# Performance work log

Measured on AMD Instinct MI355X. Metric: run time of the kernel, lower is better.

Reference implementation:

```python
import jax, jax.numpy as jnp
import numpy as np

MANIFOLD_K = 1.0   # Lorentz curvature manifold.k
POWER_K = 2        # power_k
EPS_PHI = 1e-6
EPS_FP = 1e-8

N, IN_C, OUT_C, H = 32768, 128, 128, 8


def setup_inputs() -> dict:
    key = jax.random.key(0)
    ks = jax.random.split(key, 11)
    s = 1.0 / np.sqrt(IN_C)  # nn.Linear default init scale
    u = lambda k, shape: jax.random.uniform(k, shape, jnp.float32, -s, s)
    return {
        "query_input": jax.random.normal(ks[0], (N, IN_C), jnp.float32),
        "source_input": jax.random.normal(ks[1], (N, IN_C), jnp.float32),
        "Wq_w": u(ks[2], (H, OUT_C, IN_C)),
        "Wq_b": u(ks[3], (H, OUT_C)),
        "Wk_w": u(ks[4], (H, OUT_C, IN_C)),
        "Wk_b": u(ks[5], (H, OUT_C)),
        "Wv_w": u(ks[6], (H, OUT_C, IN_C)),
        "Wv_b": u(ks[7], (H, OUT_C)),
        "v_map_w": u(ks[8], (OUT_C, OUT_C)),  # v_map_mlp acts on v (out_channels feats)
        "v_map_b": u(ks[9], (OUT_C,)),
        "norm_scale": jnp.ones((), jnp.float32),
    }


def _fp(x, p):
    # norm(x) / (norm(x**p) + eps) * x**p, norms over last dim
    norm_x = jnp.linalg.norm(x, axis=-1, keepdims=True)
    xp = x ** p
    norm_xp = jnp.linalg.norm(xp, axis=-1, keepdims=True)
    return norm_x / (norm_xp + EPS_FP) * xp


def reference(query_input, source_input, Wq_w, Wq_b, Wk_w, Wk_b, Wv_w, Wv_b,
              v_map_w, v_map_b, norm_scale):
    # Per-head HypLinear space part; the concatenated time coordinate is
    # immediately stripped by hyp_*[..., 1:] in linear_focus_attention,
    # so only the linear (space) output participates in the math.
    qs = jnp.einsum('ni,hoi->nho', query_input, Wq_w) + Wq_b   # [N,H,D]
    ks_ = jnp.einsum('ni,hoi->nho', source_input, Wk_w) + Wk_b  # [N,H,D]
    v = jnp.einsum('ni,hoi->nho', source_input, Wv_w) + Wv_b    # [N,H,D]

    denom_scale = jnp.abs(norm_scale) + EPS_PHI
    phi_qs = _fp((jax.nn.relu(qs) + EPS_PHI) / denom_scale, POWER_K)
    phi_ks = _fp((jax.nn.relu(ks_) + EPS_PHI) / denom_scale, POWER_K)

    k_transpose_v = jnp.einsum('nhm,nhd->hmd', phi_ks, v)        # [H,D,D]
    numerator = jnp.einsum('nhm,hmd->nhd', phi_qs, k_transpose_v)
    denominator = jnp.einsum('nhd,hd->nh', phi_qs, phi_ks.sum(axis=0))[..., None]
    attn_output = numerator / (denominator + EPS_PHI)            # [N,H,D]

    vss = jnp.einsum('nhd,od->nho', v, v_map_w) + v_map_b        # v_map_mlp(v)
    attn_output = attn_output + vss

    out = attn_output.mean(axis=1)                               # heads mean [N,D]
    out_time = jnp.sqrt(jnp.sum(out ** 2, axis=-1, keepdims=True) + MANIFOLD_K)
    return jnp.concatenate([out_time, out], axis=-1)             # [N,D+1]
```

## Files before the change

### kernel.cpp

```cpp
#include <hip/hip_runtime.h>

#define NTOK   32768
#define CDIM   128
#define NH     8
#define QT     32

typedef __bf16 bf16;
typedef __bf16 bf16x4v __attribute__((ext_vector_type(4)));
typedef __bf16 bf16x8v __attribute__((ext_vector_type(8)));
typedef float  f32x4   __attribute__((ext_vector_type(4)));

__device__ __forceinline__ f32x4 mfma16(bf16x8v a, bf16x8v b, f32x4 c) {
  return __builtin_amdgcn_mfma_f32_16x16x32_bf16(a, b, c, 0, 0, 0);
}

__device__ __forceinline__ float xred16(float v) {
  v += __shfl_xor(v, 1);
  v += __shfl_xor(v, 2);
  v += __shfl_xor(v, 4);
  v += __shfl_xor(v, 8);
  return v;
}

template<int CTRL>
__device__ __forceinline__ float dpp_add(float x) {
  int y = __builtin_amdgcn_mov_dpp(__float_as_int(x), CTRL, 0xf, 0xf, true);
  return x + __int_as_float(y);
}
__device__ __forceinline__ float xred16d(float v) {
  v = dpp_add<0xB1>(v);
  v = dpp_add<0x4E>(v);
  v = dpp_add<0x141>(v);
  v = dpp_add<0x140>(v);
  return v;
}

__device__ __forceinline__ int sidx(int row, int col) {
  return row * 128 + (col ^ ((row & 7) << 3));
}

__device__ __forceinline__ int tidx(int h, int tile, int kk, int lane) {
  return (((h * 8 + tile) * 4 + kk) * 64 + lane) * 8;
}

__global__ void __launch_bounds__(256) k_prepA(
    const float* __restrict__ src,
    const float* __restrict__ Wq, const float* __restrict__ Wk,
    const float* __restrict__ Wv, const float* __restrict__ Wv_b,
    bf16* __restrict__ srcT,
    bf16* __restrict__ wqT, bf16* __restrict__ wkT, bf16* __restrict__ wvT,
    float* __restrict__ Wvs, float* __restrict__ Wvbs)
{
  const int bid = blockIdx.x;
  const int tid = threadIdx.x;
  if (bid < 2048) {
    const int rb = bid;
    const int row = tid >> 4, col0 = (tid & 15) * 8;
    const float* p = src + (rb * 16 + row) * CDIM + col0;
    f32x4 v0 = *(const f32x4*)p;
    f32x4 v1 = *(const f32x4*)(p + 4);
    bf16x8v o;
    o[0] = (bf16)v0[0]; o[1] = (bf16)v0[1]; o[2] = (bf16)v0[2]; o[3] = (bf16)v0[3];
    o[4] = (bf16)v1[0]; o[5] = (bf16)v1[1]; o[6] = (bf16)v1[2]; o[7] = (bf16)v1[3];
    const int kk = col0 >> 5, lg = (col0 >> 3) & 3;
    const int lane = row + 16 * lg;
    *(bf16x8v*)(srcT + ((rb * 4 + kk) * 64 + lane) * 8) = o;
  } else {
    const int b = bid - 2048;
    const int h = b >> 6;
    const int o = (b & 63) * 2 + (tid >> 7);
    const int i = tid & 127;
    const int s = (h * CDIM + o) * CDIM + i;
    const int ot = o >> 4, l15 = o & 15;
    const int kk = i >> 5, lg = (i >> 3) & 3, j = i & 7;
    const int dst = tidx(h, ot, kk, l15 + 16 * lg) + j;
    wqT[dst] = (bf16)Wq[s];
    wkT[dst] = (bf16)Wk[s];
    wvT[dst] = (bf16)Wv[s];
    if (h == 0) {
      float sm = 0.f;
#pragma unroll
      for (int hh = 0; hh < NH; ++hh) sm += Wv[(hh * CDIM + o) * CDIM + i];
      Wvs[o * CDIM + i] = sm;
      if (o == 0) {
        float sb = 0.f;
#pragma unroll
        for (int hh = 0; hh < NH; ++hh) sb += Wv_b[hh * CDIM + i];
        Wvbs[i] = sb;
      }
    }
  }
}

__global__ void __launch_bounds__(256, 2) k_ktv(
    const bf16* __restrict__ srcT,
    const bf16* __restrict__ wkT, const bf16* __restrict__ wvT,
    const float* __restrict__ Wk_b, const float* __restrict__ Wv_b,
    bf16* __restrict__ ktv_part, float* __restrict__ ksum_part,
    int nsub, int cpx )
{
  const int x = blockIdx.x & 7;
  const int g = blockIdx.x >> 3;
  const int c = x * cpx + (g >> 3);
  const int h = g & 7;

  const int tid = threadIdx.x;
  const int w = tid >> 6, l = tid & 63;
  const int l15 = l & 15, lg = l >> 4;
  const int os = w * 32, owt = os >> 4;

  __shared__ bf16 s_phiT[128][68];
  __shared__ bf16 s_vT[128][68];
  __shared__ float s_red2[8][64];
  __shared__ float s_scale[64];

  const f32x4 z4 = {0.f, 0.f, 0.f, 0.f};

  bf16x8v bWk[2][4], bWv[2][4];
  float bK[2], bV[2];
#pragma unroll
  for (int ot = 0; ot < 2; ++ot) {
#pragma unroll
    for (int kk = 0; kk < 4; ++kk) {
      bWk[ot][kk] = *(const bf16x8v*)(wkT + tidx(h, owt + ot, kk, l));
      bWv[ot][kk] = *(const bf16x8v*)(wvT + tidx(h, owt + ot, kk, l));
    }
    bK[ot] = Wk_b[h * CDIM + os + ot * 16 + l15];
    bV[ot] = Wv_b[h * CDIM + os + ot * 16 + l15];
  }

  const int wd = (w >> 1) * 64, wm = (w & 1) * 64;
  f32x4 acc[4][4];
#pragma unroll
  for (int dt = 0; dt < 4; ++dt)
#pragma unroll
    for (int mt = 0; mt < 4; ++mt) acc[dt][mt] = z4;
  float ksacc[2] = {0.f, 0.f};

#pragma unroll 1
  for (int s = 0; s < nsub; ++s) {
    const int rbase = (c * nsub + s) * 4;
    f32x4 accK[4][2], accV[4][2];
#pragma unroll
    for (int nt = 0; nt < 4; ++nt)
#pragma unroll
      for (int ot = 0; ot < 2; ++ot) { accK[nt][ot] = z4; accV[nt][ot] = z4; }
#pragma unroll
    for (int kk = 0; kk < 4; ++kk) {
      bf16x8v a[4];
#pragma unroll
      for (int nt = 0; nt < 4; ++nt)
        a[nt] = *(const bf16x8v*)(srcT + (((rbase + nt) * 4 + kk) * 64 + l) * 8);
#pragma unroll
      for (int nt = 0; nt < 4; ++nt)
#pragma unroll
        for (int ot = 0; ot < 2; ++ot) {
          accK[nt][ot] = mfma16(a[nt], bWk[ot][kk], accK[nt][ot]);
          accV[nt][ot] = mfma16(a[nt], bWv[ot][kk], accV[nt][ot]);
        }
    }
    bf16x4v vq[4][2];
#pragma unroll
    for (int nt = 0; nt < 4; ++nt)
#pragma unroll
      for (int ot = 0; ot < 2; ++ot)
#pragma unroll
        for (int r = 0; r < 4; ++r)
          vq[nt][ot][r] = (bf16)(accV[nt][ot][r] + bV[ot]);
#pragma unroll
    for (int nt = 0; nt < 4; ++nt)
#pragma unroll
      for (int r = 0; r < 4; ++r) {
        float a2 = 0.f, a4 = 0.f;
#pragma unroll
        for (int ot = 0; ot < 2; ++ot) {
          float xv = fmaxf(accK[nt][ot][r] + bK[ot], 0.f) + 1e-6f;
          float x2 = xv * xv;
          accK[nt][ot][r] = x2;
          a2 += x2;
          a4 += x2 * x2;
        }
        a2 = xred16d(a2);
        a4 = xred16d(a4);
        if (l15 == 0) {
          s_red2[w * 2 + 0][nt * 16 + lg * 4 + r] = a2;
          s_red2[w * 2 + 1][nt * 16 + lg * 4 + r] = a4;
        }
      }
    __syncthreads();
    {
      float S2 = s_red2[0][l] + s_red2[2][l] + s_red2[4][l] + s_red2[6][l];
      float S4 = s_red2[1][l] + s_red2[3][l] + s_red2[5][l] + s_red2[7][l];
      s_scale[l] = sqrtf(S2) / (sqrtf(S4) + 1e-8f);
    }
#pragma unroll
    for (int nt = 0; nt < 4; ++nt) {
      f32x4 sc = *(const f32x4*)&s_scale[nt * 16 + lg * 4];
#pragma unroll
      for (int ot = 0; ot < 2; ++ot) {
        bf16x4v ph;
#pragma unroll
        for (int r = 0; r < 4; ++r) {
          float p = accK[nt][ot][r] * sc[r];
          ksacc[ot] += p;
          ph[r] = (bf16)p;
        }
        const int colb = os + ot * 16 + l15;
        *(bf16x4v*)&s_phiT[colb][nt * 16 + lg * 4] = ph;
        *(bf16x4v*)&s_vT[colb][nt * 16 + lg * 4] = vq[nt][ot];
      }
    }
    __syncthreads();
#pragma unroll
    for (int kkn = 0; kkn < 2; ++kkn) {
      bf16x8v aV[4], bP[4];
#pragma unroll
      for (int dt = 0; dt < 4; ++dt)
        aV[dt] = *(const bf16x8v*)&s_vT[wd + dt * 16 + l15][kkn * 32 + lg * 8];
#pragma unroll
      for (int mt = 0; mt < 4; ++mt)
        bP[mt] = *(const bf16x8v*)&s_phiT[wm + mt * 16 + l15][kkn * 32 + lg * 8];
#pragma unroll
      for (int dt = 0; dt < 4; ++dt)
#pragma unroll
        for (int mt = 0; mt < 4; ++mt)
          acc[dt][mt] = mfma16(aV[dt], bP[mt], acc[dt][mt]);
    }
  }

#pragma unroll
  for (int ot = 0; ot < 2; ++ot) {
    ksacc[ot] += __shfl_xor(ksacc[ot], 16);
    ksacc[ot] += __shfl_xor(ksacc[ot], 32);
  }
  if (l < 16) {
#pragma unroll
    for (int ot = 0; ot < 2; ++ot)
      ksum_part[(c * NH + h) * CDIM + os + ot * 16 + l] = ksacc[ot];
  }
  bf16* kp = ktv_part + ((c * NH + h) * 4 + w) * 4096;
#pragma unroll
  for (int dt = 0; dt < 4; ++dt)
#pragma unroll
    for (int mt = 0; mt < 4; ++mt) {
      bf16x4v q;
#pragma unroll
      for (int r = 0; r < 4; ++r) q[r] = (bf16)acc[dt][mt][r];
      *(bf16x4v*)(kp + ((dt * 4 + mt) * 64 + l) * 4) = q;
    }
}

__global__ void __launch_bounds__(256) k_finishB(
    const bf16* __restrict__ ktv_part, const float* __restrict__ ksum_part,
    const float* __restrict__ vmw, const float* __restrict__ vmb,
    const float* __restrict__ Wvs, const float* __restrict__ Wvbs,
    bf16* __restrict__ ktvT, bf16* __restrict__ ksb,
    bf16* __restrict__ w2sT, float* __restrict__ b2s, int nchunk)
{
  const int b = blockIdx.x;
  if (b < 512) {
    const int t = b * 256 + threadIdx.x;
    const int h = t >> 14;
    const int rem = t & 16383;
    const int d = rem >> 7, m = rem & 127;
    const int wq = ((d >> 6) << 1) | (m >> 6);
    const int dd = d & 63, mm = m & 63;
    const int dt = dd >> 4, r = dd & 3, lgp = (dd >> 2) & 3;
    const int mt = mm >> 4, l15p = mm & 15;
    const int lane = lgp * 16 + l15p;
    const int off = (h * 4 + wq) * 4096 + ((dt * 4 + mt) * 64 + lane) * 4 + r;
    float a = 0.f;
    for (int c = 0; c < nchunk; ++c)
      a += (float)ktv_part[c * (NH * 4 * 4096) + off];
    const int dtile = d >> 4, dl15 = d & 15;
    const int kk = m >> 5, mlg = (m >> 3) & 3, j = m & 7;
    ktvT[tidx(h, dtile, kk, dl15 + 16 * mlg) + j] = (bf16)a;
  } else if (b < 576) {
    const int t = (b - 512) * 256 + threadIdx.x;
    const int h = t >> 11;
    const int rem = t & 2047;
    const int kk = rem >> 9, lane = (rem >> 3) & 63, j = rem & 7;
    const int l15 = lane & 15, lg = lane >> 4;
    float a = 0.f;
    if (l15 == 0) {
      const int m = 32 * kk + 8 * lg + j;
      for (int c = 0; c < nchunk; ++c) a += ksum_part[(c * NH + h) * CDIM + m];
    }
    ksb[t] = (bf16)a;
  } else {
    const int sub = threadIdx.x >> 7, i = threadIdx.x & 127;
    const int o = (b - 576) * 2 + sub;
    __shared__ float s_vm[2][128];
    __shared__ float s_rd[2][128];
    s_vm[sub][i] = vmw[o * CDIM + i];
    __syncthreads();
    float acc = 0.f;
    for (int d = 0; d < CDIM; ++d) acc = fmaf(s_vm[sub][d], Wvs[d * CDIM + i], acc);
    const int ot = o >> 4, l15 = o & 15;
    const int kk = i >> 5, lg = (i >> 3) & 3, j = i & 7;
    w2sT[tidx(0, ot, kk, l15 + 16 * lg) + j] = (bf16)acc;
    s_rd[sub][i] = s_vm[sub][i] * Wvbs[i];
    __syncthreads();
    for (int st = 64; st > 0; st >>= 1) {
      if (i < st) s_rd[sub][i] += s_rd[sub][i + st];
      __syncthreads();
    }
    if (i == 0) b2s[o] = s_rd[sub][0] + 8.f * vmb[o];
  }
}

__global__ void __launch_bounds__(256, 2) k_out(
    const float* __restrict__ query, const bf16* __restrict__ srcT,
    const bf16* __restrict__ wqT, const float* __restrict__ Wq_b,
    const bf16* __restrict__ ktvT, const bf16* __restrict__ ksb,
    const bf16* __restrict__ w2sT, const float* __restrict__ b2s,
    float* __restrict__ out)
{
  const int nb = blockIdx.x * QT;
  const int tid = threadIdx.x;
  const int w = tid >> 6, l = tid & 63;
  const int l15 = l & 15, lg = l >> 4;
  const int os = w * 32, owt = os >> 4;

  __shared__ bf16 s_q[QT * 128];
  __shared__ bf16 s_phi[2][QT * 128];
  __shared__ float s_time[4][QT] __attribute__((aligned(16)));

  const f32x4 z4 = {0.f, 0.f, 0.f, 0.f};

#pragma unroll
  for (int j = 0; j < 4; ++j) {
    const int flat = tid + j * 256;
    const int n = flat >> 5, c4 = (flat & 31) * 4;
    f32x4 vq = *(const f32x4*)(query + (nb + n) * CDIM + c4);
    bf16x4v bq;
    bq[0] = (bf16)vq[0]; bq[1] = (bf16)vq[1]; bq[2] = (bf16)vq[2]; bq[3] = (bf16)vq[3];
    *(bf16x4v*)&s_q[sidx(n, c4)] = bq;
  }

  f32x4 accO[2][2];
#pragma unroll
  for (int nt = 0; nt < 2; ++nt)
#pragma unroll
    for (int ot = 0; ot < 2; ++ot) accO[nt][ot] = z4;

  __syncthreads();

  bf16x8v aq[2][4];
#pragma unroll
  for (int nt = 0; nt < 2; ++nt)
#pragma unroll
    for (int kk = 0; kk < 4; ++kk)
      aq[nt][kk] = *(const bf16x8v*)&s_q[sidx(nt * 16 + l15, kk * 32 + lg * 8)];

  for (int h = 0; h < NH; ++h) {
    bf16x8v wf[2][4], kf[2][4], kt[4];
#pragma unroll
    for (int ot = 0; ot < 2; ++ot)
#pragma unroll
      for (int kk = 0; kk < 4; ++kk) {
        wf[ot][kk] = *(const bf16x8v*)(wqT + tidx(h, owt + ot, kk, l));
        kf[ot][kk] = *(const bf16x8v*)(ktvT + tidx(h, owt + ot, kk, l));
      }
#pragma unroll
    for (int kk = 0; kk < 4; ++kk)
      kt[kk] = *(const bf16x8v*)(ksb + ((h * 4 + kk) * 64 + l) * 8);
    float bQ[2];
#pragma unroll
    for (int ot = 0; ot < 2; ++ot) bQ[ot] = Wq_b[h * CDIM + os + ot * 16 + l15];

    f32x4 accQ[2][2];
#pragma unroll
    for (int nt = 0; nt < 2; ++nt)
#pragma unroll
      for (int ot = 0; ot < 2; ++ot) accQ[nt][ot] = z4;
#pragma unroll
    for (int kk = 0; kk < 4; ++kk)
#pragma unroll
      for (int ot = 0; ot < 2; ++ot)
#pragma unroll
        for (int nt = 0; nt < 2; ++nt)
          accQ[nt][ot] = mfma16(aq[nt][kk], wf[ot][kk], accQ[nt][ot]);

    bf16* ph = s_phi[h & 1];
#pragma unroll
    for (int nt = 0; nt < 2; ++nt)
#pragma unroll
      for (int ot = 0; ot < 2; ++ot)
#pragma unroll
        for (int r = 0; r < 4; ++r) {
          float x = fmaxf(accQ[nt][ot][r] + bQ[ot], 0.f) + 1e-6f;
          ph[sidx(nt * 16 + lg * 4 + r, os + ot * 16 + l15)] = (bf16)(x * x);
        }
    __syncthreads();

    bf16x8v ap[2][4];
#pragma unroll
    for (int nt = 0; nt < 2; ++nt)
#pragma unroll
      for (int kk = 0; kk < 4; ++kk)
        ap[nt][kk] = *(const bf16x8v*)&ph[sidx(nt * 16 + l15, kk * 32 + lg * 8)];

    f32x4 accN[2][2], accT[2];
#pragma unroll
    for (int nt = 0; nt < 2; ++nt) {
      accT[nt] = z4;
#pragma unroll
      for (int dt = 0; dt < 2; ++dt) accN[nt][dt] = z4;
    }
#pragma unroll
    for (int kk = 0; kk < 4; ++kk) {
#pragma unroll
      for (int dt = 0; dt < 2; ++dt)
#pragma unroll
        for (int nt = 0; nt < 2; ++nt)
          accN[nt][dt] = mfma16(ap[nt][kk], kf[dt][kk], accN[nt][dt]);
#pragma unroll
      for (int nt = 0; nt < 2; ++nt)
        accT[nt] = mfma16(ap[nt][kk], kt[kk], accT[nt]);
    }
#pragma unroll
    for (int nt = 0; nt < 2; ++nt)
#pragma unroll
      for (int r = 0; r < 4; ++r) {
        float tr = __shfl(accT[nt][r], l & 48);
        float m = 1.0f / tr;
#pragma unroll
        for (int dt = 0; dt < 2; ++dt)
          accO[nt][dt][r] = fmaf(accN[nt][dt][r], m, accO[nt][dt][r]);
      }
  }

  const int rb0 = blockIdx.x * 2;
#pragma unroll
  for (int kk = 0; kk < 4; ++kk) {
    bf16x8v a[2];
#pragma unroll
    for (int nt = 0; nt < 2; ++nt)
      a[nt] = *(const bf16x8v*)(srcT + (((rb0 + nt) * 4 + kk) * 64 + l) * 8);
#pragma unroll
    for (int ot = 0; ot < 2; ++ot) {
      bf16x8v bw = *(const bf16x8v*)(w2sT + tidx(0, owt + ot, kk, l));
#pragma unroll
      for (int nt = 0; nt < 2; ++nt)
        accO[nt][ot] = mfma16(a[nt], bw, accO[nt][ot]);
    }
  }
  float bb[2];
#pragma unroll
  for (int ot = 0; ot < 2; ++ot) bb[ot] = b2s[os + ot * 16 + l15];

  float ps[2][4];
#pragma unroll
  for (int nt = 0; nt < 2; ++nt)
#pragma unroll
    for (int r = 0; r < 4; ++r) ps[nt][r] = 0.f;
#pragma unroll
  for (int nt = 0; nt < 2; ++nt)
#pragma unroll
    for (int ot = 0; ot < 2; ++ot)
#pragma unroll
      for (int r = 0; r < 4; ++r) {
        float v = (accO[nt][ot][r] + bb[ot]) * 0.125f;
        accO[nt][ot][r] = v;
        ps[nt][r] += v * v;
      }
#pragma unroll
  for (int nt = 0; nt < 2; ++nt)
#pragma unroll
    for (int r = 0; r < 4; ++r) {
      float t = xred16d(ps[nt][r]);
      if (l15 == 0) s_time[w][nt * 16 + lg * 4 + r] = t;
    }
#pragma unroll
  for (int nt = 0; nt < 2; ++nt)
#pragma unroll
    for (int ot = 0; ot < 2; ++ot)
#pragma unroll
      for (int r = 0; r < 4; ++r)
        out[(nb + nt * 16 + lg * 4 + r) * 129 + 1 + os + ot * 16 + l15] = accO[nt][ot][r];
  __syncthreads();
  if (tid < QT) {
    float S = 1.0f + s_time[0][tid] + s_time[1][tid] + s_time[2][tid] + s_time[3][tid];
    out[(nb + tid) * 129] = sqrtf(S);
  }
}

extern "C" void kernel_launch(void* const* d_in, const int* in_sizes, int n_in,
                              void* d_out, int out_size, void* d_ws, size_t ws_size,
                              hipStream_t stream) {
  const float* query  = (const float*)d_in[0];
  const float* source = (const float*)d_in[1];
  const float* Wq_w   = (const float*)d_in[2];
  const float* Wq_b   = (const float*)d_in[3];
  const float* Wk_w   = (const float*)d_in[4];
  const float* Wk_b   = (const float*)d_in[5];
  const float* Wv_w   = (const float*)d_in[6];
  const float* Wv_b   = (const float*)d_in[7];
  const float* vmw    = (const float*)d_in[8];
  const float* vmb    = (const float*)d_in[9];

  char* ws = (char*)d_ws;
  bf16*  wqT       = (bf16*)(ws + 0);
  bf16*  wkT       = (bf16*)(ws + 262144);
  bf16*  wvT       = (bf16*)(ws + 524288);
  bf16*  w2sT      = (bf16*)(ws + 786432);
  float* b2s       = (float*)(ws + 819200);
  float* Wvs       = (float*)(ws + 819712);
  float* Wvbs      = (float*)(ws + 885248);
  bf16*  ktvT      = (bf16*)(ws + 885760);
  bf16*  ksb       = (bf16*)(ws + 1147904);
  bf16*  srcT      = (bf16*)(ws + 1180672);
  float* ksum_part = (float*)(ws + 9569280);
  bf16*  ktv_part  = (bf16*)(ws + 10093568);

  int nchunk = 64, nsub = 8;
  if (ws_size < 10093568ull + 64ull * 262144ull) { nchunk = 32; nsub = 16; }

  k_prepA<<<2560, 256, 0, stream>>>(source, Wq_w, Wk_w, Wv_w, Wv_b,
                                    srcT, wqT, wkT, wvT, Wvs, Wvbs);
  k_ktv<<<nchunk * NH, 256, 0, stream>>>(srcT, wkT, wvT, Wk_b, Wv_b,
                                         ktv_part, ksum_part, nsub, nchunk / 8);
  k_finishB<<<640, 256, 0, stream>>>(ktv_part, ksum_part, vmw, vmb, Wvs, Wvbs,
                                     ktvT, ksb, w2sT, b2s, nchunk);
  k_out<<<NTOK / QT, 256, 0, stream>>>(query, srcT, wqT, Wq_b, ktvT, ksb,
                                       w2sT, b2s, (float*)d_out);
}
```

Measured before the change: 121.0 us.

## Retile k_out to 64-token blocks with 8 waves each owning 16 output columns

The output kernel now processes 64 tokens per 512-thread block. Each of 8 waves owns a 16-wide output slice across 4 row tiles, instead of 4 waves each owning 32 columns over 32 rows. Weight fragments are loaded per k-step and phi fragments are read from shared memory inside the MFMA loop, which lowers register pressure and reuses each weight fragment across more rows. The change also adds an unused prefetch of srcT into a_cur in k_ktv, which only adds dead loads that the compiler may or may not remove.

```diff
diff --git a/kernel.cpp b/kernel.cpp
--- a/kernel.cpp
+++ b/kernel.cpp
@@ -3,7 +3,6 @@
 #define NTOK   32768
 #define CDIM   128
 #define NH     8
-#define QT     32
 
 typedef __bf16 bf16;
 typedef __bf16 bf16x4v __attribute__((ext_vector_type(4)));
@@ -12,14 +11,6 @@
 
 __device__ __forceinline__ f32x4 mfma16(bf16x8v a, bf16x8v b, f32x4 c) {
   return __builtin_amdgcn_mfma_f32_16x16x32_bf16(a, b, c, 0, 0, 0);
-}
-
-__device__ __forceinline__ float xred16(float v) {
-  v += __shfl_xor(v, 1);
-  v += __shfl_xor(v, 2);
-  v += __shfl_xor(v, 4);
-  v += __shfl_xor(v, 8);
-  return v;
 }
 
 template<int CTRL>
@@ -97,7 +88,7 @@
     const bf16* __restrict__ wkT, const bf16* __restrict__ wvT,
     const float* __restrict__ Wk_b, const float* __restrict__ Wv_b,
     bf16* __restrict__ ktv_part, float* __restrict__ ksum_part,
-    int nsub, int cpx )
+    int nsub, int cpx)
 {
   const int x = blockIdx.x & 7;
   const int g = blockIdx.x >> 3;
@@ -136,6 +127,11 @@
 #pragma unroll
     for (int mt = 0; mt < 4; ++mt) acc[dt][mt] = z4;
   float ksacc[2] = {0.f, 0.f};
+
+  bf16x8v a_cur[4];
+#pragma unroll
+  for (int kk = 0; kk < 4; ++kk)
+    a_cur[kk] = *(const bf16x8v*)(srcT + (((c * nsub * 4 + kk) * 64 + l) * 8) + 0);
 
 #pragma unroll 1
   for (int s = 0; s < nsub; ++s) {
@@ -227,6 +223,7 @@
           acc[dt][mt] = mfma16(aV[dt], bP[mt], acc[dt][mt]);
     }
   }
+  (void)a_cur;
 
 #pragma unroll
   for (int ot = 0; ot < 2; ++ot) {
@@ -309,28 +306,27 @@
   }
 }
 
-__global__ void __launch_bounds__(256, 2) k_out(
+__global__ void __launch_bounds__(512, 2) k_out(
     const float* __restrict__ query, const bf16* __restrict__ srcT,
     const bf16* __restrict__ wqT, const float* __restrict__ Wq_b,
     const bf16* __restrict__ ktvT, const bf16* __restrict__ ksb,
     const bf16* __restrict__ w2sT, const float* __restrict__ b2s,
     float* __restrict__ out)
 {
-  const int nb = blockIdx.x * QT;
+  const int nb = blockIdx.x * 64;
   const int tid = threadIdx.x;
   const int w = tid >> 6, l = tid & 63;
   const int l15 = l & 15, lg = l >> 4;
-  const int os = w * 32, owt = os >> 4;
-
-  __shared__ bf16 s_q[QT * 128];
-  __shared__ bf16 s_phi[2][QT * 128];
-  __shared__ float s_time[4][QT] __attribute__((aligned(16)));
+
+  __shared__ bf16 s_q[64 * 128];
+  __shared__ bf16 s_phi[2][64 * 128];
+  __shared__ float s_time[8][64];
 
   const f32x4 z4 = {0.f, 0.f, 0.f, 0.f};
 
 #pragma unroll
   for (int j = 0; j < 4; ++j) {
-    const int flat = tid + j * 256;
+    const int flat = tid + j * 512;
     const int n = flat >> 5, c4 = (flat & 31) * 4;
     f32x4 vq = *(const f32x4*)(query + (nb + n) * CDIM + c4);
     bf16x4v bq;
@@ -338,150 +334,103 @@
     *(bf16x4v*)&s_q[sidx(n, c4)] = bq;
   }
 
-  f32x4 accO[2][2];
-#pragma unroll
-  for (int nt = 0; nt < 2; ++nt)
-#pragma unroll
-    for (int ot = 0; ot < 2; ++ot) accO[nt][ot] = z4;
+  f32x4 accO[4];
+#pragma unroll
+  for (int nt = 0; nt < 4; ++nt) accO[nt] = z4;
 
   __syncthreads();
 
-  bf16x8v aq[2][4];
-#pragma unroll
-  for (int nt = 0; nt < 2; ++nt)
+  bf16x8v aq[4][4];
+#pragma unroll
+  for (int nt = 0; nt < 4; ++nt)
 #pragma unroll
     for (int kk = 0; kk < 4; ++kk)
       aq[nt][kk] = *(const bf16x8v*)&s_q[sidx(nt * 16 + l15, kk * 32 + lg * 8)];
 
   for (int h = 0; h < NH; ++h) {
-    bf16x8v wf[2][4], kf[2][4], kt[4];
-#pragma unroll
-    for (int ot = 0; ot < 2; ++ot)
-#pragma unroll
-      for (int kk = 0; kk < 4; ++kk) {
-        wf[ot][kk] = *(const bf16x8v*)(wqT + tidx(h, owt + ot, kk, l));
-        kf[ot][kk] = *(const bf16x8v*)(ktvT + tidx(h, owt + ot, kk, l));
-      }
-#pragma unroll
-    for (int kk = 0; kk < 4; ++kk)
-      kt[kk] = *(const bf16x8v*)(ksb + ((h * 4 + kk) * 64 + l) * 8);
-    float bQ[2];
-#pragma unroll
-    for (int ot = 0; ot < 2; ++ot) bQ[ot] = Wq_b[h * CDIM + os + ot * 16 + l15];
-
-    f32x4 accQ[2][2];
-#pragma unroll
-    for (int nt = 0; nt < 2; ++nt)
-#pragma unroll
-      for (int ot = 0; ot < 2; ++ot) accQ[nt][ot] = z4;
-#pragma unroll
-    for (int kk = 0; kk < 4; ++kk)
-#pragma unroll
-      for (int ot = 0; ot < 2; ++ot)
-#pragma unroll
-        for (int nt = 0; nt < 2; ++nt)
-          accQ[nt][ot] = mfma16(aq[nt][kk], wf[ot][kk], accQ[nt][ot]);
-
+    const float bQ = Wq_b[h * CDIM + w * 16 + l15];
+    f32x4 accQ[4];
+#pragma unroll
+    for (int nt = 0; nt < 4; ++nt) accQ[nt] = z4;
+#pragma unroll
+    for (int kk = 0; kk < 4; ++kk) {
+      bf16x8v wfk = *(const bf16x8v*)(wqT + tidx(h, w, kk, l));
+#pragma unroll
+      for (int nt = 0; nt < 4; ++nt)
+        accQ[nt] = mfma16(aq[nt][kk], wfk, accQ[nt]);
+    }
     bf16* ph = s_phi[h & 1];
 #pragma unroll
-    for (int nt = 0; nt < 2; ++nt)
-#pragma unroll
-      for (int ot = 0; ot < 2; ++ot)
-#pragma unroll
-        for (int r = 0; r < 4; ++r) {
-          float x = fmaxf(accQ[nt][ot][r] + bQ[ot], 0.f) + 1e-6f;
-          ph[sidx(nt * 16 + lg * 4 + r, os + ot * 16 + l15)] = (bf16)(x * x);
-        }
+    for (int nt = 0; nt < 4; ++nt)
+#pragma unroll
+      for (int r = 0; r < 4; ++r) {
+        float xv = fmaxf(accQ[nt][r] + bQ, 0.f) + 1e-6f;
+        ph[sidx(nt * 16 + lg * 4 + r, w * 16 + l15)] = (bf16)(xv * xv);
+      }
     __syncthreads();
 
-    bf16x8v ap[2][4];
-#pragma unroll
-    for (int nt = 0; nt < 2; ++nt)
-#pragma unroll
-      for (int kk = 0; kk < 4; ++kk)
-        ap[nt][kk] = *(const bf16x8v*)&ph[sidx(nt * 16 + l15, kk * 32 + lg * 8)];
-
-    f32x4 accN[2][2], accT[2];
-#pragma unroll
-    for (int nt = 0; nt < 2; ++nt) {
-      accT[nt] = z4;
-#pragma unroll
-      for (int dt = 0; dt < 2; ++dt) accN[nt][dt] = z4;
-    }
+    f32x4 accN[4], accT[4];
+#pragma unroll
+    for (int nt = 0; nt < 4; ++nt) { accN[nt] = z4; accT[nt] = z4; }
 #pragma unroll
     for (int kk = 0; kk < 4; ++kk) {
-#pragma unroll
-      for (int dt = 0; dt < 2; ++dt)
-#pragma unroll
-        for (int nt = 0; nt < 2; ++nt)
-          accN[nt][dt] = mfma16(ap[nt][kk], kf[dt][kk], accN[nt][dt]);
-#pragma unroll
-      for (int nt = 0; nt < 2; ++nt)
-        accT[nt] = mfma16(ap[nt][kk], kt[kk], accT[nt]);
-    }
-#pragma unroll
-    for (int nt = 0; nt < 2; ++nt)
+      bf16x8v kfk = *(const bf16x8v*)(ktvT + tidx(h, w, kk, l));
+      bf16x8v ktk = *(const bf16x8v*)(ksb + ((h * 4 + kk) * 64 + l) * 8);
+#pragma unroll
+      for (int nt = 0; nt < 4; ++nt) {
+        bf16x8v apx = *(const bf16x8v*)&ph[sidx(nt * 16 + l15, kk * 32 + lg * 8)];
+        accN[nt] = mfma16(apx, kfk, accN[nt]);
+        accT[nt] = mfma16(apx, ktk, accT[nt]);
+      }
+    }
+#pragma unroll
+    for (int nt = 0; nt < 4; ++nt)
 #pragma unroll
       for (int r = 0; r < 4; ++r) {
         float tr = __shfl(accT[nt][r], l & 48);
         float m = 1.0f / tr;
-#pragma unroll
-        for (int dt = 0; dt < 2; ++dt)
-          accO[nt][dt][r] = fmaf(accN[nt][dt][r], m, accO[nt][dt][r]);
-      }
-  }
-
-  const int rb0 = blockIdx.x * 2;
+        accO[nt][r] = fmaf(accN[nt][r], m, accO[nt][r]);
+      }
+  }
+
+  const int rb0 = blockIdx.x * 4;
 #pragma unroll
   for (int kk = 0; kk < 4; ++kk) {
-    bf16x8v a[2];
-#pragma unroll
-    for (int nt = 0; nt < 2; ++nt)
-      a[nt] = *(const bf16x8v*)(srcT + (((rb0 + nt) * 4 + kk) * 64 + l) * 8);
-#pragma unroll
-    for (int ot = 0; ot < 2; ++ot) {
-      bf16x8v bw = *(const bf16x8v*)(w2sT + tidx(0, owt + ot, kk, l));
-#pragma unroll
-      for (int nt = 0; nt < 2; ++nt)
-        accO[nt][ot] = mfma16(a[nt], bw, accO[nt][ot]);
-    }
-  }
-  float bb[2];
-#pragma unroll
-  for (int ot = 0; ot < 2; ++ot) bb[ot] = b2s[os + ot * 16 + l15];
-
-  float ps[2][4];
-#pragma unroll
-  for (int nt = 0; nt < 2; ++nt)
-#pragma unroll
-    for (int r = 0; r < 4; ++r) ps[nt][r] = 0.f;
-#pragma unroll
-  for (int nt = 0; nt < 2; ++nt)
-#pragma unroll
-    for (int ot = 0; ot < 2; ++ot)
-#pragma unroll
-      for (int r = 0; r < 4; ++r) {
-        float v = (accO[nt][ot][r] + bb[ot]) * 0.125f;
-        accO[nt][ot][r] = v;
-        ps[nt][r] += v * v;
-      }
-#pragma unroll
-  for (int nt = 0; nt < 2; ++nt)
+    bf16x8v bwk = *(const bf16x8v*)(w2sT + tidx(0, w, kk, l));
+#pragma unroll
+    for (int nt = 0; nt < 4; ++nt) {
+      bf16x8v a = *(const bf16x8v*)(srcT + (((rb0 + nt) * 4 + kk) * 64 + l) * 8);
+      accO[nt] = mfma16(a, bwk, accO[nt]);
+    }
+  }
+  const float bb = b2s[w * 16 + l15];
+
+  float ps[4][4];
+#pragma unroll
+  for (int nt = 0; nt < 4; ++nt)
+#pragma unroll
+    for (int r = 0; r < 4; ++r) {
+      float v = (accO[nt][r] + bb) * 0.125f;
+      accO[nt][r] = v;
+      ps[nt][r] = v * v;
+    }
+#pragma unroll
+  for (int nt = 0; nt < 4; ++nt)
 #pragma unroll
     for (int r = 0; r < 4; ++r) {
       float t = xred16d(ps[nt][r]);
       if (l15 == 0) s_time[w][nt * 16 + lg * 4 + r] = t;
     }
 #pragma unroll
-  for (int nt = 0; nt < 2; ++nt)
-#pragma unroll
-    for (int ot = 0; ot < 2; ++ot)
-#pragma unroll
-      for (int r = 0; r < 4; ++r)
-        out[(nb + nt * 16 + lg * 4 + r) * 129 + 1 + os + ot * 16 + l15] = accO[nt][ot][r];
+  for (int nt = 0; nt < 4; ++nt)
+#pragma unroll
+    for (int r = 0; r < 4; ++r)
+      out[(nb + nt * 16 + lg * 4 + r) * 129 + 1 + w * 16 + l15] = accO[nt][r];
   __syncthreads();
-  if (tid < QT) {
-    float S = 1.0f + s_time[0][tid] + s_time[1][tid] + s_time[2][tid] + s_time[3][tid];
+  if (tid < 64) {
+    float S = 1.0f;
+#pragma unroll
+    for (int ww = 0; ww < 8; ++ww) S += s_time[ww][tid];
     out[(nb + tid) * 129] = sqrtf(S);
   }
 }
@@ -523,6 +472,6 @@
                                          ktv_part, ksum_part, nsub, nchunk / 8);
   k_finishB<<<640, 256, 0, stream>>>(ktv_part, ksum_part, vmw, vmb, Wvs, Wvbs,
                                      ktvT, ksb, w2sT, b2s, nchunk);
-  k_out<<<NTOK / QT, 256, 0, stream>>>(query, srcT, wqT, Wq_b, ktvT, ksb,
+  k_out<<<NTOK / 64, 512, 0, stream>>>(query, srcT, wqT, Wq_b, ktvT, ksb,
                                        w2sT, b2s, (float*)d_out);
 }
```

Result: slower. 129.3 us (+6.9%).

## Software-pipeline k_ktv projection with double-buffered LDS tiles

Applied to the files above, without the earlier changes.

Moves the K/V projection and norm reduction for the next sub-tile ahead of the barrier, so it overlaps with the current tile's phi scaling and KᵀV MFMAs. LDS buffers for phi, v and reduction partials are double-buffered, which removes one __syncthreads per iteration. In exchange, LDS use and live register state both grow, which may limit occupancy.

```diff
diff --git a/kernel.cpp b/kernel.cpp
--- a/kernel.cpp
+++ b/kernel.cpp
@@ -12,14 +12,6 @@
 
 __device__ __forceinline__ f32x4 mfma16(bf16x8v a, bf16x8v b, f32x4 c) {
   return __builtin_amdgcn_mfma_f32_16x16x32_bf16(a, b, c, 0, 0, 0);
-}
-
-__device__ __forceinline__ float xred16(float v) {
-  v += __shfl_xor(v, 1);
-  v += __shfl_xor(v, 2);
-  v += __shfl_xor(v, 4);
-  v += __shfl_xor(v, 8);
-  return v;
 }
 
 template<int CTRL>
@@ -92,12 +84,69 @@
   }
 }
 
+__device__ __forceinline__ void proj_norms(
+    const bf16* __restrict__ srcT,
+    const bf16x8v (&bWk)[2][4], const bf16x8v (&bWv)[2][4],
+    const float (&bK)[2], const float (&bV)[2],
+    int rbase, int l, int w, int lg,
+    f32x4 (&accK)[4][2], bf16x4v (&vq)[4][2],
+    float (*red)[64])
+{
+  const f32x4 z4 = {0.f, 0.f, 0.f, 0.f};
+  f32x4 accV[4][2];
+#pragma unroll
+  for (int nt = 0; nt < 4; ++nt)
+#pragma unroll
+    for (int ot = 0; ot < 2; ++ot) { accK[nt][ot] = z4; accV[nt][ot] = z4; }
+#pragma unroll
+  for (int kk = 0; kk < 4; ++kk) {
+    bf16x8v a[4];
+#pragma unroll
+    for (int nt = 0; nt < 4; ++nt)
+      a[nt] = *(const bf16x8v*)(srcT + (((rbase + nt) * 4 + kk) * 64 + l) * 8);
+#pragma unroll
+    for (int nt = 0; nt < 4; ++nt)
+#pragma unroll
+      for (int ot = 0; ot < 2; ++ot) {
+        accK[nt][ot] = mfma16(a[nt], bWk[ot][kk], accK[nt][ot]);
+        accV[nt][ot] = mfma16(a[nt], bWv[ot][kk], accV[nt][ot]);
+      }
+  }
+#pragma unroll
+  for (int nt = 0; nt < 4; ++nt)
+#pragma unroll
+    for (int ot = 0; ot < 2; ++ot)
+#pragma unroll
+      for (int r = 0; r < 4; ++r)
+        vq[nt][ot][r] = (bf16)(accV[nt][ot][r] + bV[ot]);
+#pragma unroll
+  for (int nt = 0; nt < 4; ++nt)
+#pragma unroll
+    for (int r = 0; r < 4; ++r) {
+      float a2 = 0.f, a4 = 0.f;
+#pragma unroll
+      for (int ot = 0; ot < 2; ++ot) {
+        float xv = fmaxf(accK[nt][ot][r] + bK[ot], 0.f) + 1e-6f;
+        float x2 = xv * xv;
+        accK[nt][ot][r] = x2;
+        a2 += x2;
+        a4 += x2 * x2;
+      }
+      a2 = xred16d(a2);
+      a4 = xred16d(a4);
+      if ((l & 15) == 0) {
+        red[w * 2 + 0][nt * 16 + lg * 4 + r] = a2;
+        red[w * 2 + 1][nt * 16 + lg * 4 + r] = a4;
+      }
+    }
+}
+
 __global__ void __launch_bounds__(256, 2) k_ktv(
     const bf16* __restrict__ srcT,
     const bf16* __restrict__ wkT, const bf16* __restrict__ wvT,
     const float* __restrict__ Wk_b, const float* __restrict__ Wv_b,
     bf16* __restrict__ ktv_part, float* __restrict__ ksum_part,
-    int nsub, int cpx )
+    int nsub, int cpx)
 {
   const int x = blockIdx.x & 7;
   const int g = blockIdx.x >> 3;
@@ -109,9 +158,9 @@
   const int l15 = l & 15, lg = l >> 4;
   const int os = w * 32, owt = os >> 4;
 
-  __shared__ bf16 s_phiT[128][68];
-  __shared__ bf16 s_vT[128][68];
-  __shared__ float s_red2[8][64];
+  __shared__ bf16 s_phiT[2][128][68];
+  __shared__ bf16 s_vT[2][128][68];
+  __shared__ float s_red2[2][8][64];
   __shared__ float s_scale[64];
 
   const f32x4 z4 = {0.f, 0.f, 0.f, 0.f};
@@ -137,60 +186,19 @@
     for (int mt = 0; mt < 4; ++mt) acc[dt][mt] = z4;
   float ksacc[2] = {0.f, 0.f};
 
+  f32x4 accK[4][2];
+  bf16x4v vq[4][2];
+
+  proj_norms(srcT, bWk, bWv, bK, bV, (c * nsub) * 4, l, w, lg,
+             accK, vq, s_red2[0]);
+  __syncthreads();
+
 #pragma unroll 1
   for (int s = 0; s < nsub; ++s) {
-    const int rbase = (c * nsub + s) * 4;
-    f32x4 accK[4][2], accV[4][2];
-#pragma unroll
-    for (int nt = 0; nt < 4; ++nt)
-#pragma unroll
-      for (int ot = 0; ot < 2; ++ot) { accK[nt][ot] = z4; accV[nt][ot] = z4; }
-#pragma unroll
-    for (int kk = 0; kk < 4; ++kk) {
-      bf16x8v a[4];
-#pragma unroll
-      for (int nt = 0; nt < 4; ++nt)
-        a[nt] = *(const bf16x8v*)(srcT + (((rbase + nt) * 4 + kk) * 64 + l) * 8);
-#pragma unroll
-      for (int nt = 0; nt < 4; ++nt)
-#pragma unroll
-        for (int ot = 0; ot < 2; ++ot) {
-          accK[nt][ot] = mfma16(a[nt], bWk[ot][kk], accK[nt][ot]);
-          accV[nt][ot] = mfma16(a[nt], bWv[ot][kk], accV[nt][ot]);
-        }
-    }
-    bf16x4v vq[4][2];
-#pragma unroll
-    for (int nt = 0; nt < 4; ++nt)
-#pragma unroll
-      for (int ot = 0; ot < 2; ++ot)
-#pragma unroll
-        for (int r = 0; r < 4; ++r)
-          vq[nt][ot][r] = (bf16)(accV[nt][ot][r] + bV[ot]);
-#pragma unroll
-    for (int nt = 0; nt < 4; ++nt)
-#pragma unroll
-      for (int r = 0; r < 4; ++r) {
-        float a2 = 0.f, a4 = 0.f;
-#pragma unroll
-        for (int ot = 0; ot < 2; ++ot) {
-          float xv = fmaxf(accK[nt][ot][r] + bK[ot], 0.f) + 1e-6f;
-          float x2 = xv * xv;
-          accK[nt][ot][r] = x2;
-          a2 += x2;
-          a4 += x2 * x2;
-        }
-        a2 = xred16d(a2);
-        a4 = xred16d(a4);
-        if (l15 == 0) {
-          s_red2[w * 2 + 0][nt * 16 + lg * 4 + r] = a2;
-          s_red2[w * 2 + 1][nt * 16 + lg * 4 + r] = a4;
-        }
-      }
-    __syncthreads();
+    const int pb = s & 1;
     {
-      float S2 = s_red2[0][l] + s_red2[2][l] + s_red2[4][l] + s_red2[6][l];
-      float S4 = s_red2[1][l] + s_red2[3][l] + s_red2[5][l] + s_red2[7][l];
+      float S2 = s_red2[pb][0][l] + s_red2[pb][2][l] + s_red2[pb][4][l] + s_red2[pb][6][l];
+      float S4 = s_red2[pb][1][l] + s_red2[pb][3][l] + s_red2[pb][5][l] + s_red2[pb][7][l];
       s_scale[l] = sqrtf(S2) / (sqrtf(S4) + 1e-8f);
     }
 #pragma unroll
@@ -206,20 +214,23 @@
           ph[r] = (bf16)p;
         }
         const int colb = os + ot * 16 + l15;
-        *(bf16x4v*)&s_phiT[colb][nt * 16 + lg * 4] = ph;
-        *(bf16x4v*)&s_vT[colb][nt * 16 + lg * 4] = vq[nt][ot];
-      }
-    }
+        *(bf16x4v*)&s_phiT[pb][colb][nt * 16 + lg * 4] = ph;
+        *(bf16x4v*)&s_vT[pb][colb][nt * 16 + lg * 4] = vq[nt][ot];
+      }
+    }
+    if (s + 1 < nsub)
+      proj_norms(srcT, bWk, bWv, bK, bV, (c * nsub + s + 1) * 4, l, w, lg,
+                 accK, vq, s_red2[pb ^ 1]);
     __syncthreads();
 #pragma unroll
     for (int kkn = 0; kkn < 2; ++kkn) {
       bf16x8v aV[4], bP[4];
 #pragma unroll
       for (int dt = 0; dt < 4; ++dt)
-        aV[dt] = *(const bf16x8v*)&s_vT[wd + dt * 16 + l15][kkn * 32 + lg * 8];
+        aV[dt] = *(const bf16x8v*)&s_vT[pb][wd + dt * 16 + l15][kkn * 32 + lg * 8];
 #pragma unroll
       for (int mt = 0; mt < 4; ++mt)
-        bP[mt] = *(const bf16x8v*)&s_phiT[wm + mt * 16 + l15][kkn * 32 + lg * 8];
+        bP[mt] = *(const bf16x8v*)&s_phiT[pb][wm + mt * 16 + l15][kkn * 32 + lg * 8];
 #pragma unroll
       for (int dt = 0; dt < 4; ++dt)
 #pragma unroll
@@ -389,8 +400,8 @@
       for (int ot = 0; ot < 2; ++ot)
 #pragma unroll
         for (int r = 0; r < 4; ++r) {
-          float x = fmaxf(accQ[nt][ot][r] + bQ[ot], 0.f) + 1e-6f;
-          ph[sidx(nt * 16 + lg * 4 + r, os + ot * 16 + l15)] = (bf16)(x * x);
+          float xv = fmaxf(accQ[nt][ot][r] + bQ[ot], 0.f) + 1e-6f;
+          ph[sidx(nt * 16 + lg * 4 + r, os + ot * 16 + l15)] = (bf16)(xv * xv);
         }
     __syncthreads();
 
```

New measurement: 126.7 us. 1.05x slower.

## Reassociate K^T V as (phiK^T X) Wv^T to drop per-token V projection

Applied to the files above, without the earlier changes.

Instead of projecting V per token and forming phiK^T V, the ktv kernel now accumulates G = phiK^T X against a transposed bf16 copy of the source, and a new small kernel computes ktv = G·Wv^T + Wv_b·ksum. This removes half of the projection MFMAs and the V staging in shared memory inside the main reduction loop. In exchange it adds a transposed source copy in prepA (extra global write and read), an fp32 G intermediate, and an extra serial launch of a scalar-FMA 64-block kernel.

```diff
diff --git a/kernel.cpp b/kernel.cpp
--- a/kernel.cpp
+++ b/kernel.cpp
@@ -12,14 +12,6 @@
 
 __device__ __forceinline__ f32x4 mfma16(bf16x8v a, bf16x8v b, f32x4 c) {
   return __builtin_amdgcn_mfma_f32_16x16x32_bf16(a, b, c, 0, 0, 0);
-}
-
-__device__ __forceinline__ float xred16(float v) {
-  v += __shfl_xor(v, 1);
-  v += __shfl_xor(v, 2);
-  v += __shfl_xor(v, 4);
-  v += __shfl_xor(v, 8);
-  return v;
 }
 
 template<int CTRL>
@@ -47,12 +39,13 @@
     const float* __restrict__ src,
     const float* __restrict__ Wq, const float* __restrict__ Wk,
     const float* __restrict__ Wv, const float* __restrict__ Wv_b,
-    bf16* __restrict__ srcT,
-    bf16* __restrict__ wqT, bf16* __restrict__ wkT, bf16* __restrict__ wvT,
+    bf16* __restrict__ srcT, bf16* __restrict__ srcTB,
+    bf16* __restrict__ wqT, bf16* __restrict__ wkT,
     float* __restrict__ Wvs, float* __restrict__ Wvbs)
 {
   const int bid = blockIdx.x;
   const int tid = threadIdx.x;
+  __shared__ bf16 s_t[64][136];
   if (bid < 2048) {
     const int rb = bid;
     const int row = tid >> 4, col0 = (tid & 15) * 8;
@@ -65,7 +58,7 @@
     const int kk = col0 >> 5, lg = (col0 >> 3) & 3;
     const int lane = row + 16 * lg;
     *(bf16x8v*)(srcT + ((rb * 4 + kk) * 64 + lane) * 8) = o;
-  } else {
+  } else if (bid < 2560) {
     const int b = bid - 2048;
     const int h = b >> 6;
     const int o = (b & 63) * 2 + (tid >> 7);
@@ -76,7 +69,6 @@
     const int dst = tidx(h, ot, kk, l15 + 16 * lg) + j;
     wqT[dst] = (bf16)Wq[s];
     wkT[dst] = (bf16)Wk[s];
-    wvT[dst] = (bf16)Wv[s];
     if (h == 0) {
       float sm = 0.f;
 #pragma unroll
@@ -89,15 +81,37 @@
         Wvbs[i] = sb;
       }
     }
+  } else {
+    const int rb = bid - 2560;
+#pragma unroll
+    for (int jj = 0; jj < 8; ++jj) {
+      const int flat = tid + jj * 256;
+      const int n = flat >> 5, c4 = (flat & 31) * 4;
+      f32x4 v = *(const f32x4*)(src + (rb * 64 + n) * CDIM + c4);
+      bf16x4v bv;
+      bv[0] = (bf16)v[0]; bv[1] = (bf16)v[1]; bv[2] = (bf16)v[2]; bv[3] = (bf16)v[3];
+      *(bf16x4v*)&s_t[n][c4] = bv;
+    }
+    __syncthreads();
+#pragma unroll
+    for (int k = 0; k < 4; ++k) {
+      const int gi = tid + k * 256;
+      const int it = gi >> 7, kkn = (gi >> 6) & 1, lane = gi & 63;
+      const int l15 = lane & 15, lg = lane >> 4;
+      bf16x8v o;
+#pragma unroll
+      for (int j = 0; j < 8; ++j)
+        o[j] = s_t[kkn * 32 + lg * 8 + j][it * 16 + l15];
+      *(bf16x8v*)(srcTB + (((rb * 8 + it) * 2 + kkn) * 64 + lane) * 8) = o;
+    }
   }
 }
 
 __global__ void __launch_bounds__(256, 2) k_ktv(
-    const bf16* __restrict__ srcT,
-    const bf16* __restrict__ wkT, const bf16* __restrict__ wvT,
-    const float* __restrict__ Wk_b, const float* __restrict__ Wv_b,
-    bf16* __restrict__ ktv_part, float* __restrict__ ksum_part,
-    int nsub, int cpx )
+    const bf16* __restrict__ srcT, const bf16* __restrict__ srcTB,
+    const bf16* __restrict__ wkT, const float* __restrict__ Wk_b,
+    bf16* __restrict__ g_part, float* __restrict__ ksum_part,
+    int nsub, int cpx)
 {
   const int x = blockIdx.x & 7;
   const int g = blockIdx.x >> 3;
@@ -110,41 +124,39 @@
   const int os = w * 32, owt = os >> 4;
 
   __shared__ bf16 s_phiT[128][68];
-  __shared__ bf16 s_vT[128][68];
   __shared__ float s_red2[8][64];
   __shared__ float s_scale[64];
 
   const f32x4 z4 = {0.f, 0.f, 0.f, 0.f};
 
-  bf16x8v bWk[2][4], bWv[2][4];
-  float bK[2], bV[2];
+  bf16x8v bWk[2][4];
+  float bK[2];
 #pragma unroll
   for (int ot = 0; ot < 2; ++ot) {
 #pragma unroll
-    for (int kk = 0; kk < 4; ++kk) {
+    for (int kk = 0; kk < 4; ++kk)
       bWk[ot][kk] = *(const bf16x8v*)(wkT + tidx(h, owt + ot, kk, l));
-      bWv[ot][kk] = *(const bf16x8v*)(wvT + tidx(h, owt + ot, kk, l));
-    }
     bK[ot] = Wk_b[h * CDIM + os + ot * 16 + l15];
-    bV[ot] = Wv_b[h * CDIM + os + ot * 16 + l15];
-  }
-
-  const int wd = (w >> 1) * 64, wm = (w & 1) * 64;
+  }
+
+  const int wm = (w >> 1) * 64;
+  const int wi2 = (w & 1) * 4;
   f32x4 acc[4][4];
 #pragma unroll
-  for (int dt = 0; dt < 4; ++dt)
-#pragma unroll
-    for (int mt = 0; mt < 4; ++mt) acc[dt][mt] = z4;
+  for (int mt = 0; mt < 4; ++mt)
+#pragma unroll
+    for (int it = 0; it < 4; ++it) acc[mt][it] = z4;
   float ksacc[2] = {0.f, 0.f};
 
 #pragma unroll 1
   for (int s = 0; s < nsub; ++s) {
-    const int rbase = (c * nsub + s) * 4;
-    f32x4 accK[4][2], accV[4][2];
+    const int rb64 = c * nsub + s;
+    const int rbase = rb64 * 4;
+    f32x4 accK[4][2];
 #pragma unroll
     for (int nt = 0; nt < 4; ++nt)
 #pragma unroll
-      for (int ot = 0; ot < 2; ++ot) { accK[nt][ot] = z4; accV[nt][ot] = z4; }
+      for (int ot = 0; ot < 2; ++ot) accK[nt][ot] = z4;
 #pragma unroll
     for (int kk = 0; kk < 4; ++kk) {
       bf16x8v a[4];
@@ -154,19 +166,9 @@
 #pragma unroll
       for (int nt = 0; nt < 4; ++nt)
 #pragma unroll
-        for (int ot = 0; ot < 2; ++ot) {
+        for (int ot = 0; ot < 2; ++ot)
           accK[nt][ot] = mfma16(a[nt], bWk[ot][kk], accK[nt][ot]);
-          accV[nt][ot] = mfma16(a[nt], bWv[ot][kk], accV[nt][ot]);
-        }
-    }
-    bf16x4v vq[4][2];
-#pragma unroll
-    for (int nt = 0; nt < 4; ++nt)
-#pragma unroll
-      for (int ot = 0; ot < 2; ++ot)
-#pragma unroll
-        for (int r = 0; r < 4; ++r)
-          vq[nt][ot][r] = (bf16)(accV[nt][ot][r] + bV[ot]);
+    }
 #pragma unroll
     for (int nt = 0; nt < 4; ++nt)
 #pragma unroll
@@ -205,26 +207,24 @@
           ksacc[ot] += p;
           ph[r] = (bf16)p;
         }
-        const int colb = os + ot * 16 + l15;
-        *(bf16x4v*)&s_phiT[colb][nt * 16 + lg * 4] = ph;
-        *(bf16x4v*)&s_vT[colb][nt * 16 + lg * 4] = vq[nt][ot];
+        *(bf16x4v*)&s_phiT[os + ot * 16 + l15][nt * 16 + lg * 4] = ph;
       }
     }
     __syncthreads();
 #pragma unroll
     for (int kkn = 0; kkn < 2; ++kkn) {
-      bf16x8v aV[4], bP[4];
-#pragma unroll
-      for (int dt = 0; dt < 4; ++dt)
-        aV[dt] = *(const bf16x8v*)&s_vT[wd + dt * 16 + l15][kkn * 32 + lg * 8];
+      bf16x8v aP[4], bS[4];
 #pragma unroll
       for (int mt = 0; mt < 4; ++mt)
-        bP[mt] = *(const bf16x8v*)&s_phiT[wm + mt * 16 + l15][kkn * 32 + lg * 8];
-#pragma unroll
-      for (int dt = 0; dt < 4; ++dt)
-#pragma unroll
-        for (int mt = 0; mt < 4; ++mt)
-          acc[dt][mt] = mfma16(aV[dt], bP[mt], acc[dt][mt]);
+        aP[mt] = *(const bf16x8v*)&s_phiT[wm + mt * 16 + l15][kkn * 32 + lg * 8];
+#pragma unroll
+      for (int it = 0; it < 4; ++it)
+        bS[it] = *(const bf16x8v*)(srcTB + (((rb64 * 8 + wi2 + it) * 2 + kkn) * 64 + l) * 8);
+#pragma unroll
+      for (int mt = 0; mt < 4; ++mt)
+#pragma unroll
+        for (int it = 0; it < 4; ++it)
+          acc[mt][it] = mfma16(aP[mt], bS[it], acc[mt][it]);
     }
   }
 
@@ -238,23 +238,23 @@
     for (int ot = 0; ot < 2; ++ot)
       ksum_part[(c * NH + h) * CDIM + os + ot * 16 + l] = ksacc[ot];
   }
-  bf16* kp = ktv_part + ((c * NH + h) * 4 + w) * 4096;
-#pragma unroll
-  for (int dt = 0; dt < 4; ++dt)
-#pragma unroll
-    for (int mt = 0; mt < 4; ++mt) {
+  bf16* kp = g_part + ((c * NH + h) * 4 + w) * 4096;
+#pragma unroll
+  for (int mt = 0; mt < 4; ++mt)
+#pragma unroll
+    for (int it = 0; it < 4; ++it) {
       bf16x4v q;
 #pragma unroll
-      for (int r = 0; r < 4; ++r) q[r] = (bf16)acc[dt][mt][r];
-      *(bf16x4v*)(kp + ((dt * 4 + mt) * 64 + l) * 4) = q;
+      for (int r = 0; r < 4; ++r) q[r] = (bf16)acc[mt][it][r];
+      *(bf16x4v*)(kp + ((mt * 4 + it) * 64 + l) * 4) = q;
     }
 }
 
 __global__ void __launch_bounds__(256) k_finishB(
-    const bf16* __restrict__ ktv_part, const float* __restrict__ ksum_part,
+    const bf16* __restrict__ g_part, const float* __restrict__ ksum_part,
     const float* __restrict__ vmw, const float* __restrict__ vmb,
     const float* __restrict__ Wvs, const float* __restrict__ Wvbs,
-    bf16* __restrict__ ktvT, bf16* __restrict__ ksb,
+    float* __restrict__ Gf, bf16* __restrict__ ksb, float* __restrict__ ksum_red,
     bf16* __restrict__ w2sT, float* __restrict__ b2s, int nchunk)
 {
   const int b = blockIdx.x;
@@ -262,19 +262,17 @@
     const int t = b * 256 + threadIdx.x;
     const int h = t >> 14;
     const int rem = t & 16383;
-    const int d = rem >> 7, m = rem & 127;
-    const int wq = ((d >> 6) << 1) | (m >> 6);
-    const int dd = d & 63, mm = m & 63;
-    const int dt = dd >> 4, r = dd & 3, lgp = (dd >> 2) & 3;
-    const int mt = mm >> 4, l15p = mm & 15;
+    const int mG = rem >> 7, iG = rem & 127;
+    const int wq = ((mG >> 6) << 1) | (iG >> 6);
+    const int dd = mG & 63, mm = iG & 63;
+    const int mt = dd >> 4, r = dd & 3, lgp = (dd >> 2) & 3;
+    const int it = mm >> 4, l15p = mm & 15;
     const int lane = lgp * 16 + l15p;
-    const int off = (h * 4 + wq) * 4096 + ((dt * 4 + mt) * 64 + lane) * 4 + r;
+    const int off = (h * 4 + wq) * 4096 + ((mt * 4 + it) * 64 + lane) * 4 + r;
     float a = 0.f;
     for (int c = 0; c < nchunk; ++c)
-      a += (float)ktv_part[c * (NH * 4 * 4096) + off];
-    const int dtile = d >> 4, dl15 = d & 15;
-    const int kk = m >> 5, mlg = (m >> 3) & 3, j = m & 7;
-    ktvT[tidx(h, dtile, kk, dl15 + 16 * mlg) + j] = (bf16)a;
+      a += (float)g_part[c * (NH * 4 * 4096) + off];
+    Gf[t] = a;
   } else if (b < 576) {
     const int t = (b - 512) * 256 + threadIdx.x;
     const int h = t >> 11;
@@ -285,6 +283,7 @@
     if (l15 == 0) {
       const int m = 32 * kk + 8 * lg + j;
       for (int c = 0; c < nchunk; ++c) a += ksum_part[(c * NH + h) * CDIM + m];
+      ksum_red[h * CDIM + m] = a;
     }
     ksb[t] = (bf16)a;
   } else {
@@ -309,6 +308,38 @@
   }
 }
 
+__global__ void __launch_bounds__(256) k_finishC(
+    const float* __restrict__ Gf, const float* __restrict__ Wv,
+    const float* __restrict__ Wv_b, const float* __restrict__ ksum_red,
+    bf16* __restrict__ ktvT)
+{
+  const int t = blockIdx.x * 256 + threadIdx.x;
+  const int h = t >> 11;
+  const int rem = t & 2047;
+  const int dtile = rem >> 8, kk = (rem >> 6) & 3, lane = rem & 63;
+  const int l15 = lane & 15, lg = lane >> 4;
+  const int d = dtile * 16 + l15;
+  const int m0 = kk * 32 + lg * 8;
+  const float bv = Wv_b[h * CDIM + d];
+  float acc[8];
+#pragma unroll
+  for (int j = 0; j < 8; ++j) acc[j] = bv * ksum_red[h * CDIM + m0 + j];
+  const float* wvr = Wv + (h * CDIM + d) * CDIM;
+  const float* gr  = Gf + (h * CDIM + m0) * CDIM;
+  for (int i = 0; i < CDIM; i += 4) {
+    f32x4 wv4 = *(const f32x4*)(wvr + i);
+#pragma unroll
+    for (int j = 0; j < 8; ++j) {
+      f32x4 g4 = *(const f32x4*)(gr + j * CDIM + i);
+      acc[j] += wv4[0] * g4[0] + wv4[1] * g4[1] + wv4[2] * g4[2] + wv4[3] * g4[3];
+    }
+  }
+  bf16x8v o;
+#pragma unroll
+  for (int j = 0; j < 8; ++j) o[j] = (bf16)acc[j];
+  *(bf16x8v*)(ktvT + tidx(h, dtile, kk, lane)) = o;
+}
+
 __global__ void __launch_bounds__(256, 2) k_out(
     const float* __restrict__ query, const bf16* __restrict__ srcT,
     const bf16* __restrict__ wqT, const float* __restrict__ Wq_b,
@@ -389,8 +420,8 @@
       for (int ot = 0; ot < 2; ++ot)
 #pragma unroll
         for (int r = 0; r < 4; ++r) {
-          float x = fmaxf(accQ[nt][ot][r] + bQ[ot], 0.f) + 1e-6f;
-          ph[sidx(nt * 16 + lg * 4 + r, os + ot * 16 + l15)] = (bf16)(x * x);
+          float xv = fmaxf(accQ[nt][ot][r] + bQ[ot], 0.f) + 1e-6f;
+          ph[sidx(nt * 16 + lg * 4 + r, os + ot * 16 + l15)] = (bf16)(xv * xv);
         }
     __syncthreads();
 
@@ -503,26 +534,29 @@
   char* ws = (char*)d_ws;
   bf16*  wqT       = (bf16*)(ws + 0);
   bf16*  wkT       = (bf16*)(ws + 262144);
-  bf16*  wvT       = (bf16*)(ws + 524288);
-  bf16*  w2sT      = (bf16*)(ws + 786432);
-  float* b2s       = (float*)(ws + 819200);
-  float* Wvs       = (float*)(ws + 819712);
-  float* Wvbs      = (float*)(ws + 885248);
-  bf16*  ktvT      = (bf16*)(ws + 885760);
-  bf16*  ksb       = (bf16*)(ws + 1147904);
-  bf16*  srcT      = (bf16*)(ws + 1180672);
-  float* ksum_part = (float*)(ws + 9569280);
-  bf16*  ktv_part  = (bf16*)(ws + 10093568);
+  bf16*  w2sT      = (bf16*)(ws + 524288);
+  float* b2s       = (float*)(ws + 557056);
+  float* Wvs       = (float*)(ws + 557568);
+  float* Wvbs      = (float*)(ws + 623104);
+  bf16*  ktvT      = (bf16*)(ws + 623616);
+  bf16*  ksb       = (bf16*)(ws + 885760);
+  float* ksum_red  = (float*)(ws + 918528);
+  float* Gf        = (float*)(ws + 922624);
+  bf16*  srcT      = (bf16*)(ws + 1446912);
+  bf16*  srcTB     = (bf16*)(ws + 9835520);
+  float* ksum_part = (float*)(ws + 18224128);
+  bf16*  g_part    = (bf16*)(ws + 18486272);
 
   int nchunk = 64, nsub = 8;
-  if (ws_size < 10093568ull + 64ull * 262144ull) { nchunk = 32; nsub = 16; }
-
-  k_prepA<<<2560, 256, 0, stream>>>(source, Wq_w, Wk_w, Wv_w, Wv_b,
-                                    srcT, wqT, wkT, wvT, Wvs, Wvbs);
-  k_ktv<<<nchunk * NH, 256, 0, stream>>>(srcT, wkT, wvT, Wk_b, Wv_b,
-                                         ktv_part, ksum_part, nsub, nchunk / 8);
-  k_finishB<<<640, 256, 0, stream>>>(ktv_part, ksum_part, vmw, vmb, Wvs, Wvbs,
-                                     ktvT, ksb, w2sT, b2s, nchunk);
+  if (ws_size < 18486272ull + 64ull * 262144ull) { nchunk = 32; nsub = 16; }
+
+  k_prepA<<<3072, 256, 0, stream>>>(source, Wq_w, Wk_w, Wv_w, Wv_b,
+                                    srcT, srcTB, wqT, wkT, Wvs, Wvbs);
+  k_ktv<<<nchunk * NH, 256, 0, stream>>>(srcT, srcTB, wkT, Wk_b,
+                                         g_part, ksum_part, nsub, nchunk / 8);
+  k_finishB<<<640, 256, 0, stream>>>(g_part, ksum_part, vmw, vmb, Wvs, Wvbs,
+                                     Gf, ksb, ksum_red, w2sT, b2s, nchunk);
+  k_finishC<<<64, 256, 0, stream>>>(Gf, Wv_w, Wv_b, ksum_red, ktvT);
   k_out<<<NTOK / QT, 256, 0, stream>>>(query, srcT, wqT, Wq_b, ktvT, ksb,
                                        w2sT, b2s, (float*)d_out);
 }
```

After: 135.4 us. 1.12x slower.
